# Kernel optimization log

Hardware: AMD Instinct MI355X
Metric: run time of the kernel (lower is better)

Reference implementation:

```python
import jax, jax.numpy as jnp
import numpy as np

N_HEAD = 4
D_K = 512 // N_HEAD  # 128
PAD = 5  # (kernel 11 - 1) // 2, sanm_shift=0 -> symmetric 'same' padding
EPS = 1e-5


def layer_norm(x, w, b):
    m = jnp.mean(x, axis=-1, keepdims=True)
    v = jnp.mean(jnp.square(x - m), axis=-1, keepdims=True)
    return (x - m) * jax.lax.rsqrt(v + EPS) * w + b


def setup_inputs() -> dict:
    key = jax.random.key(0)
    ks = jax.random.split(key, 8)
    B, T, D = 64, 218, 512
    s = 0.05
    return {
        "x": jax.random.normal(ks[0], (B, T, D), jnp.float32),
        "masks": jnp.ones((B, T), jnp.float32),
        "ln0_w": jax.random.uniform(ks[1], (D,), jnp.float32, 0.9, 1.1),
        "ln0_b": jnp.zeros((D,), jnp.float32),
        "ln1_w": jax.random.uniform(ks[2], (D,), jnp.float32, 0.9, 1.1),
        "ln1_b": jnp.zeros((D,), jnp.float32),
        "qkv_w": jax.random.normal(ks[3], (D, 3 * D), jnp.float32) * s,
        "qkv_b": jnp.zeros((3 * D,), jnp.float32),
        "out_w": jax.random.normal(ks[4], (D, D), jnp.float32) * s,
        "out_b": jnp.zeros((D,), jnp.float32),
        "fsmn_w": jax.random.normal(ks[5], (D, D, 11), jnp.float32) * s,
        "w1": jax.random.normal(ks[6], (D, 4 * D), jnp.float32) * s,
        "b1": jnp.zeros((4 * D,), jnp.float32),
        "w2": jax.random.normal(ks[7], (4 * D, D), jnp.float32) * s,
        "b2": jnp.zeros((D,), jnp.float32),
    }


def encoder_layer(x, masks, ln0_w, ln0_b, ln1_w, ln1_b, qkv_w, qkv_b,
                  out_w, out_b, fsmn_w, w1, b1, w2, b2):
    B, T, D = x.shape
    m = masks[..., None]  # (B,T,1)

    # ---- self_attn_sanm block ----
    residual = x
    h = layer_norm(x, ln0_w, ln0_b)
    qkv = h @ qkv_w + qkv_b                      # (B,T,3D)
    q, k, v = jnp.split(qkv, 3, axis=-1)         # each (B,T,D)

    # FSMN memory branch on (masked) v: Conv1d(512,512,11), 'same' padding
    vm = v * m
    # torch conv weight (out,in,k) -> jax 'WIO' kernel (k,in,out)
    kern = jnp.transpose(fsmn_w, (2, 1, 0))
    fsmn = jax.lax.conv_general_dilated(
        vm, kern, window_strides=(1,), padding=[(PAD, PAD)],
        dimension_numbers=("NWC", "WIO", "NWC"))
    fsmn = (fsmn + vm) * m                       # (B,T,D)

    # multi-head attention
    def heads(t):  # (B,T,D) -> (B,H,T,dk)
        return t.reshape(B, T, N_HEAD, D_K).transpose(0, 2, 1, 3)
    qh, kh, vh = heads(q), heads(k), heads(v)
    scores = jnp.einsum("bhqd,bhkd->bhqk", qh, kh) / np.sqrt(D_K)
    neg = jnp.finfo(scores.dtype).min
    scores = jnp.where(masks[:, None, None, :] > 0, scores, neg)
    attn = jax.nn.softmax(scores, axis=-1)
    ctx = jnp.einsum("bhqk,bhkd->bhqd", attn, vh)
    ctx = ctx.transpose(0, 2, 1, 3).reshape(B, T, D)
    att_out = ctx @ out_w + out_b + fsmn
    x = residual + att_out

    # ---- feed-forward block (512 -> 2048 -> 512, relu) ----
    residual = x
    h = layer_norm(x, ln1_w, ln1_b)
    ffn = jax.nn.relu(h @ w1 + b1) @ w2 + b2
    return residual + ffn


def reference(x, masks, ln0_w, ln0_b, ln1_w, ln1_b, qkv_w, qkv_b,
              out_w, out_b, fsmn_w, w1, b1, w2, b2):
    return encoder_layer(x, masks, ln0_w, ln0_b, ln1_w, ln1_b,
                         qkv_w, qkv_b, out_w, out_b, fsmn_w, w1, b1, w2, b2)
```

## Files before the change

kernel.cpp:

```cpp
#include <hip/hip_runtime.h>
#include <cstdint>

#define B_   64
#define T_   218
#define TP_  228
#define D_   512
#define M_   13952
#define MT_  109
#define H_   4
#define DK_  128
#define N3_  1536
#define DFF_ 2048
#define KC_  5632

typedef unsigned short u16;
using short8 = __attribute__((ext_vector_type(8))) short;
using f32x4  = __attribute__((ext_vector_type(4))) float;

__device__ __forceinline__ float b2f(u16 u) {
  union { float f; uint32_t i; } v; v.i = ((uint32_t)u) << 16; return v.f;
}
__device__ __forceinline__ u16 f2b(float f) {
  union { float f; uint32_t i; } v; v.f = f;
  uint32_t r = v.i + 0x7fffu + ((v.i >> 16) & 1u);
  return (u16)(r >> 16);
}
union U8 { uint4 v; u16 u[8]; };

__device__ __forceinline__ void gll16(const u16* g, u16* l) {
  __builtin_amdgcn_global_load_lds(
      (const __attribute__((address_space(1))) unsigned int*)g,
      (__attribute__((address_space(3))) unsigned int*)l, 16, 0, 0);
}


template<int MODE>
__global__ __launch_bounds__(256, 2)
void gemm_u(const u16* __restrict__ A, int sA, const u16* __restrict__ Bt, int sB,
            const float* __restrict__ bias, const u16* __restrict__ convb,
            u16* __restrict__ vmout,
            const float* __restrict__ add_f, void* __restrict__ outp,
            int N, int K, int ntc, const float* __restrict__ masks)
{
  __shared__ u16 As[128 * 32];
  __shared__ u16 Bs[128 * 32];

  const int xcd = blockIdx.x & 7;
  const int lin = blockIdx.x >> 3;
  const int nt = lin % ntc;
  const int mt = xcd + 8 * (lin / ntc);
  if (mt >= MT_) return;
  const int m0 = mt * 128, n0 = nt * 128;

  const int tid = threadIdx.x, lane = tid & 63, w = tid >> 6;
  const int wm = (w >> 1) * 64, wn = (w & 1) * 64;
  const int l15 = lane & 15, qd = lane >> 4;

  const int rl = lane >> 2;
  const int ce = ((lane & 3) ^ ((lane >> 3) & 3)) * 8;
  const int sw8 = (qd ^ ((lane >> 1) & 3)) * 8;
  const int r0 = m0 + w * 16 + rl, r1 = r0 + 64;
  const u16* ag0 = A + (size_t)r0 * sA + ce;
  const u16* ag1 = A + (size_t)r1 * sA + ce;
  const u16* bg0 = Bt + (size_t)(n0 + w * 16 + rl) * sB + ce;
  const u16* bg1 = bg0 + (size_t)64 * sB;
  u16* lA0 = As + w * 512;
  u16* lA1 = As + 2048 + w * 512;
  u16* lB0 = Bs + w * 512;
  u16* lB1 = Bs + 2048 + w * 512;

  const f32x4 z4 = {0.f, 0.f, 0.f, 0.f};
  f32x4 acc[4][4];
#pragma unroll
  for (int i = 0; i < 4; i++)
#pragma unroll
    for (int j = 0; j < 4; j++) acc[i][j] = z4;

  for (int k0 = 0; k0 < K; k0 += 32) {
    __syncthreads();
    gll16(ag0 + k0, lA0);
    gll16(ag1 + k0, lA1);
    gll16(bg0 + k0, lB0);
    gll16(bg1 + k0, lB1);
    __syncthreads();
    short8 af[4], bf[4];
#pragma unroll
    for (int mi = 0; mi < 4; mi++) af[mi] = *(const short8*)&As[(wm + mi * 16 + l15) * 32 + sw8];
#pragma unroll
    for (int ni = 0; ni < 4; ni++) bf[ni] = *(const short8*)&Bs[(wn + ni * 16 + l15) * 32 + sw8];
#pragma unroll
    for (int mi = 0; mi < 4; mi++)
#pragma unroll
      for (int ni = 0; ni < 4; ni++)
        acc[mi][ni] = __builtin_amdgcn_mfma_f32_16x16x32_bf16(af[mi], bf[ni], acc[mi][ni], 0, 0, 0);
  }

#pragma unroll
  for (int ni = 0; ni < 4; ni++) {
    const int c = n0 + wn + ni * 16 + l15;
    const float bv = bias[c];
#pragma unroll
    for (int mi = 0; mi < 4; mi++) {
#pragma unroll
      for (int rg = 0; rg < 4; rg++) {
        const int r = m0 + wm + mi * 16 + qd * 4 + rg;
        float v = acc[mi][ni][rg] + bv;
        if (MODE == 0) {
          ((u16*)outp)[(size_t)r * N + c] = f2b(v);
          if (c >= 1024) {
            const int b = r / T_, t = r - b * T_;
            vmout[((size_t)b * TP_ + t + 5) * D_ + (c - 1024)] = f2b(v * masks[r]);
          }
        } else if (MODE == 1) {
          const size_t idx = (size_t)r * N + c;
          ((float*)outp)[idx] = v + b2f(convb[idx]) + add_f[idx];
        } else if (MODE == 2) {
          ((u16*)outp)[(size_t)r * N + c] = f2b(fmaxf(v, 0.f));
        } else {
          const size_t idx = (size_t)r * N + c;
          ((float*)outp)[idx] = v + add_f[idx];
        }
      }
    }
  }
}

__global__ __launch_bounds__(256, 2)
void conv_gemm(const u16* __restrict__ vmpad, const u16* __restrict__ Wt,
               const float* __restrict__ masks, u16* __restrict__ convb)
{
  __shared__ u16 As[240 * 32];
  __shared__ u16 Bs[11 * 64 * 32];

  const int nt = blockIdx.x & 7, b = blockIdx.x >> 3;
  const int n0 = nt * 64;
  const int base = b * TP_;

  const int tid = threadIdx.x, lane = tid & 63, w = tid >> 6;
  const int wm = (w >> 1) * 112, wn = (w & 1) * 32;
  const int l15 = lane & 15, qd = lane >> 4;
  const int rl = lane >> 2;
  const int ce = ((lane & 3) ^ ((lane >> 3) & 3)) * 8;

  int abase[7];
#pragma unroll
  for (int mi = 0; mi < 7; mi++) abase[mi] = (wm + mi * 16 + l15) * 64;
  int toff[11];
#pragma unroll
  for (int tap = 0; tap < 11; tap++)
    toff[tap] = tap * 64 + ((qd ^ (((l15 + tap) >> 1) & 3)) << 4);
  const int swb8 = (qd ^ ((l15 >> 1) & 3)) * 8;

  const f32x4 z4 = {0.f, 0.f, 0.f, 0.f};
  f32x4 acc[7][2];
#pragma unroll
  for (int i = 0; i < 7; i++) { acc[i][0] = z4; acc[i][1] = z4; }

  for (int kc = 0; kc < 16; kc++) {
    const int kb = kc * 32;
    __syncthreads();
    for (int c = w; c < 15; c += 4)
      gll16(vmpad + (size_t)(base + c * 16 + rl) * D_ + kb + ce, As + c * 512);
    for (int c = w; c < 44; c += 4) {
      const int tap = c >> 2, q = c & 3;
      gll16(Wt + (size_t)(n0 + q * 16 + rl) * KC_ + tap * 512 + kb + ce,
            Bs + c * 512);
    }
    __syncthreads();
    const char* Ab = (const char*)As;
#pragma unroll
    for (int tap = 0; tap < 11; tap++) {
      short8 bf0 = *(const short8*)&Bs[tap * 2048 + (wn + l15) * 32 + swb8];
      short8 bf1 = *(const short8*)&Bs[tap * 2048 + (wn + 16 + l15) * 32 + swb8];
#pragma unroll
      for (int mi = 0; mi < 7; mi++) {
        short8 af = *(const short8*)(Ab + (abase[mi] + toff[tap]));
        acc[mi][0] = __builtin_amdgcn_mfma_f32_16x16x32_bf16(af, bf0, acc[mi][0], 0, 0, 0);
        acc[mi][1] = __builtin_amdgcn_mfma_f32_16x16x32_bf16(af, bf1, acc[mi][1], 0, 0, 0);
      }
    }
  }

#pragma unroll
  for (int mi = 0; mi < 7; mi++) {
#pragma unroll
    for (int rg = 0; rg < 4; rg++) {
      const int rlcl = wm + mi * 16 + qd * 4 + rg;
      if (rlcl < T_) {
        const int r = b * T_ + rlcl;
        const int vrow = base + rlcl + 5;
        const float m = masks[r];
#pragma unroll
        for (int ni = 0; ni < 2; ni++) {
          const int c = n0 + wn + ni * 16 + l15;
          const float vm = b2f(vmpad[(size_t)vrow * D_ + c]);
          convb[(size_t)r * D_ + c] = f2b((acc[mi][ni][rg] + vm) * m);
        }
      }
    }
  }
}

__global__ __launch_bounds__(256, 2)
void attn_fused(const u16* __restrict__ qkv, const float* __restrict__ masks,
                u16* __restrict__ ctx)
{
  __shared__ u16 smem[29696];
  __shared__ float red0[4][64];
  __shared__ float red1[4][64];
  u16* Qs = smem;
  u16* Ks = smem + 64 * 136;
  u16* Ps = smem;
  u16* Vs = smem + 64 * 232;

  const int tid = threadIdx.x, lane = tid & 63, w = tid >> 6;
  const int l15 = lane & 15, qd = lane >> 4;
  const int bh = blockIdx.y, b = bh >> 2, h = bh & 3;
  const int q0 = blockIdx.x * 64;
  const uint4 uz = make_uint4(0, 0, 0, 0);

#pragma unroll
  for (int i = 0; i < 4; i++) {
    const int ch = tid + i * 256;
    const int row = ch >> 4, cg = (ch & 15) * 8;
    const int t = q0 + row;
    uint4 v = uz;
    if (t < T_) v = *(const uint4*)(qkv + ((size_t)b * T_ + t) * N3_ + h * DK_ + cg);
    *(uint4*)&Qs[row * 136 + cg] = v;
  }

  const f32x4 z4 = {0.f, 0.f, 0.f, 0.f};
  f32x4 acc[4][4];
#pragma unroll
  for (int i = 0; i < 4; i++)
#pragma unroll
    for (int j = 0; j < 4; j++) acc[i][j] = z4;

#pragma unroll
  for (int kc = 0; kc < 4; kc++) {
    __syncthreads();
#pragma unroll
    for (int i = 0; i < 4; i++) {
      const int ch = tid + i * 256;
      const int row = ch >> 4, cg = (ch & 15) * 8;
      const int t = kc * 64 + row;
      uint4 v = uz;
      if (t < T_) v = *(const uint4*)(qkv + ((size_t)b * T_ + t) * N3_ + D_ + h * DK_ + cg);
      *(uint4*)&Ks[row * 136 + cg] = v;
    }
    __syncthreads();
#pragma unroll
    for (int ks = 0; ks < 4; ks++) {
      short8 bf = *(const short8*)&Ks[(w * 16 + l15) * 136 + ks * 32 + qd * 8];
#pragma unroll
      for (int mi = 0; mi < 4; mi++) {
        short8 af = *(const short8*)&Qs[(mi * 16 + l15) * 136 + ks * 32 + qd * 8];
        acc[kc][mi] = __builtin_amdgcn_mfma_f32_16x16x32_bf16(af, bf, acc[kc][mi], 0, 0, 0);
      }
    }
  }

  const float scale = 0.08838834764831845f;
  const int colb = w * 16 + l15;
  bool valid[4];
#pragma unroll
  for (int kc = 0; kc < 4; kc++) {
    const int col = kc * 64 + colb;
    valid[kc] = (col < T_) && (masks[b * T_ + col] > 0.f);
  }

  float mx[4][4];
#pragma unroll
  for (int mi = 0; mi < 4; mi++)
#pragma unroll
    for (int rg = 0; rg < 4; rg++) {
      float m = -1e30f;
#pragma unroll
      for (int kc = 0; kc < 4; kc++)
        if (valid[kc]) m = fmaxf(m, acc[kc][mi][rg] * scale);
      for (int d = 1; d < 16; d <<= 1) m = fmaxf(m, __shfl_xor(m, d, 64));
      mx[mi][rg] = m;
    }
  if (l15 == 0) {
#pragma unroll
    for (int mi = 0; mi < 4; mi++)
#pragma unroll
      for (int rg = 0; rg < 4; rg++) red0[w][mi * 16 + qd * 4 + rg] = mx[mi][rg];
  }
  __syncthreads();
#pragma unroll
  for (int mi = 0; mi < 4; mi++)
#pragma unroll
    for (int rg = 0; rg < 4; rg++) {
      const int r = mi * 16 + qd * 4 + rg;
      mx[mi][rg] = fmaxf(fmaxf(red0[0][r], red0[1][r]), fmaxf(red0[2][r], red0[3][r]));
    }
  float sm[4][4];
#pragma unroll
  for (int mi = 0; mi < 4; mi++)
#pragma unroll
    for (int rg = 0; rg < 4; rg++) {
      float s = 0.f;
#pragma unroll
      for (int kc = 0; kc < 4; kc++)
        if (valid[kc]) s += __expf(acc[kc][mi][rg] * scale - mx[mi][rg]);
      for (int d = 1; d < 16; d <<= 1) s += __shfl_xor(s, d, 64);
      sm[mi][rg] = s;
    }
  if (l15 == 0) {
#pragma unroll
    for (int mi = 0; mi < 4; mi++)
#pragma unroll
      for (int rg = 0; rg < 4; rg++) red1[w][mi * 16 + qd * 4 + rg] = sm[mi][rg];
  }
  __syncthreads();
#pragma unroll
  for (int mi = 0; mi < 4; mi++)
#pragma unroll
    for (int rg = 0; rg < 4; rg++) {
      const int r = mi * 16 + qd * 4 + rg;
      const float inv = 1.f / (red1[0][r] + red1[1][r] + red1[2][r] + red1[3][r]);
#pragma unroll
      for (int kc = 0; kc < 4; kc++) {
        const int col = kc * 64 + colb;
        if (col < 224) {
          const float p = valid[kc] ? __expf(acc[kc][mi][rg] * scale - mx[mi][rg]) * inv : 0.f;
          Ps[r * 232 + col] = f2b(p);
        }
      }
    }

  const int kvg = tid >> 4, dg = tid & 15;
#pragma unroll
  for (int half = 0; half < 2; ++half) {
    __syncthreads();
#pragma unroll
    for (int r = 0; r < 14; ++r) {
      const int kv = r * 16 + kvg;
      ushort4 vv = make_ushort4(0, 0, 0, 0);
      if (kv < T_)
        vv = *(const ushort4*)(qkv + ((size_t)b * T_ + kv) * N3_ + 1024 + h * DK_ + half * 64 + dg * 4);
      Vs[(dg * 4 + 0) * 232 + kv] = vv.x;
      Vs[(dg * 4 + 1) * 232 + kv] = vv.y;
      Vs[(dg * 4 + 2) * 232 + kv] = vv.z;
      Vs[(dg * 4 + 3) * 232 + kv] = vv.w;
    }
    __syncthreads();
    f32x4 a2[4] = {z4, z4, z4, z4};
#pragma unroll
    for (int k0 = 0; k0 < 7; ++k0) {
      short8 af = *(const short8*)&Ps[(w * 16 + l15) * 232 + k0 * 32 + qd * 8];
#pragma unroll
      for (int nt = 0; nt < 4; ++nt) {
        short8 bf = *(const short8*)&Vs[(nt * 16 + l15) * 232 + k0 * 32 + qd * 8];
        a2[nt] = __builtin_amdgcn_mfma_f32_16x16x32_bf16(af, bf, a2[nt], 0, 0, 0);
      }
    }
    const int tb = q0 + w * 16 + qd * 4;
#pragma unroll
    for (int nt = 0; nt < 4; ++nt) {
      const int d = h * DK_ + half * 64 + nt * 16 + l15;
#pragma unroll
      for (int rg = 0; rg < 4; ++rg) {
        const int tt = tb + rg;
        if (tt < T_) ctx[((size_t)b * T_ + tt) * D_ + d] = f2b(a2[nt][rg]);
      }
    }
  }
}

__global__ __launch_bounds__(256)
void ln_k(const float* __restrict__ x, const float* __restrict__ wgt,
          const float* __restrict__ bia, u16* __restrict__ outp)
{
  const int lane = threadIdx.x & 63, wv = threadIdx.x >> 6;
  const size_t row = (size_t)blockIdx.x * 4 + wv;
  const float* rp = x + row * D_ + lane * 8;
  float v[8], s = 0.f, s2 = 0.f;
  float4 r0 = *(const float4*)rp;
  float4 r1 = *(const float4*)(rp + 4);
  v[0] = r0.x; v[1] = r0.y; v[2] = r0.z; v[3] = r0.w;
  v[4] = r1.x; v[5] = r1.y; v[6] = r1.z; v[7] = r1.w;
#pragma unroll
  for (int i = 0; i < 8; i++) { s += v[i]; s2 += v[i] * v[i]; }
  for (int d = 1; d < 64; d <<= 1) { s += __shfl_xor(s, d, 64); s2 += __shfl_xor(s2, d, 64); }
  const float mean = s * (1.f / 512.f);
  const float var  = s2 * (1.f / 512.f) - mean * mean;
  const float rs   = rsqrtf(var + 1e-5f);
  float4 w0 = *(const float4*)(wgt + lane * 8);
  float4 w1 = *(const float4*)(wgt + lane * 8 + 4);
  float4 b0 = *(const float4*)(bia + lane * 8);
  float4 b1 = *(const float4*)(bia + lane * 8 + 4);
  const float wv8[8] = {w0.x, w0.y, w0.z, w0.w, w1.x, w1.y, w1.z, w1.w};
  const float bv8[8] = {b0.x, b0.y, b0.z, b0.w, b1.x, b1.y, b1.z, b1.w};
  U8 o;
#pragma unroll
  for (int i = 0; i < 8; i++)
    o.u[i] = f2b((v[i] - mean) * rs * wv8[i] + bv8[i]);
  *(uint4*)(outp + row * D_ + lane * 8) = o.v;
}

__global__ __launch_bounds__(256)
void prep_all(const float* __restrict__ qkv_w, const float* __restrict__ out_w,
              const float* __restrict__ w1, const float* __restrict__ w2,
              const float* __restrict__ fsmn_w,
              u16* __restrict__ qkv_wT, u16* __restrict__ out_wT,
              u16* __restrict__ w1T, u16* __restrict__ w2T,
              u16* __restrict__ fsmnW2, u16* __restrict__ vmpad)
{
  const int bid = blockIdx.x;
  if (bid < 3072) {
    const float* src; u16* dst; int K, N, tb;
    if (bid < 768)       { src = qkv_w; dst = qkv_wT; K = 512;  N = 1536; tb = bid; }
    else if (bid < 1024) { src = out_w; dst = out_wT; K = 512;  N = 512;  tb = bid - 768; }
    else if (bid < 2048) { src = w1;    dst = w1T;    K = 512;  N = 2048; tb = bid - 1024; }
    else                 { src = w2;    dst = w2T;    K = 2048; N = 512;  tb = bid - 2048; }
    const int ktiles = K / 32;
    const int k0 = (tb % ktiles) * 32, n0 = (tb / ktiles) * 32;
    __shared__ float tile[32][33];
    const int x = threadIdx.x & 31, y = threadIdx.x >> 5;
#pragma unroll
    for (int j = 0; j < 4; j++)
      tile[y + j * 8][x] = src[(size_t)(k0 + y + j * 8) * N + n0 + x];
    __syncthreads();
#pragma unroll
    for (int j = 0; j < 4; j++)
      dst[(size_t)(n0 + y + j * 8) * K + k0 + x] = f2b(tile[x][y + j * 8]);
  } else if (bid < 4096) {
    const int idx = (bid - 3072) * 256 + threadIdx.x;
    const int o = idx >> 9, i = idx & 511;
    const float* s = fsmn_w + (size_t)idx * 11;
#pragma unroll
    for (int tap = 0; tap < 11; ++tap)
      fsmnW2[(size_t)o * KC_ + tap * 512 + i] = f2b(s[tap]);
  } else {
    const int e8 = (bid - 4096) * 256 + threadIdx.x;
    const int e  = e8 * 8;
    const int c  = e & 511;
    const int pr = e >> 9;
    int row;
    if (pr < 640) {
      const int b = pr / 10, j = pr % 10;
      row = b * TP_ + ((j < 5) ? j : (218 + j));
    } else {
      row = B_ * TP_ + (pr - 640);
    }
    *(uint4*)(vmpad + (size_t)row * D_ + c) = make_uint4(0, 0, 0, 0);
  }
}

extern "C" void kernel_launch(void* const* d_in, const int* in_sizes, int n_in,
                              void* d_out, int out_size, void* d_ws, size_t ws_size,
                              hipStream_t stream)
{
  const float* x      = (const float*)d_in[0];
  const float* masks  = (const float*)d_in[1];
  const float* ln0_w  = (const float*)d_in[2];
  const float* ln0_b  = (const float*)d_in[3];
  const float* ln1_w  = (const float*)d_in[4];
  const float* ln1_b  = (const float*)d_in[5];
  const float* qkv_w  = (const float*)d_in[6];
  const float* qkv_b  = (const float*)d_in[7];
  const float* out_w  = (const float*)d_in[8];
  const float* out_b  = (const float*)d_in[9];
  const float* fsmn_w = (const float*)d_in[10];
  const float* w1     = (const float*)d_in[11];
  const float* b1     = (const float*)d_in[12];
  const float* w2     = (const float*)d_in[13];
  const float* b2     = (const float*)d_in[14];
  float* outp = (float*)d_out;
  u16* ws   = (u16*)d_ws;

  size_t off = 0;
  u16* qkv_wT = ws + off; off += (size_t)1536 * 512;
  u16* out_wT = ws + off; off += (size_t)512 * 512;
  u16* w1T    = ws + off; off += (size_t)2048 * 512;
  u16* w2T    = ws + off; off += (size_t)512 * 2048;
  u16* fsmnW2 = ws + off; off += (size_t)512 * KC_;
  u16* slotA  = ws + off; off += (size_t)M_ * 512;
  u16* qkvb   = ws + off; off += (size_t)M_ * 1536;
  u16* vmpad  = ws + off; off += (size_t)(B_ * TP_ + 320) * 512;
  u16* regionX= ws + off;
  u16* convb  = regionX;
  u16* hid    = regionX;
  u16* h1     = qkvb;
  float* x1   = (float*)(qkvb + (size_t)M_ * 512);

  prep_all<<<4126, 256, 0, stream>>>(qkv_w, out_w, w1, w2, fsmn_w,
                                     qkv_wT, out_wT, w1T, w2T, fsmnW2, vmpad);
  ln_k<<<M_ / 4, 256, 0, stream>>>(x, ln0_w, ln0_b, slotA);
  gemm_u<0><<<8 * 14 * 12, 256, 0, stream>>>(
      slotA, 512, qkv_wT, 512, qkv_b, nullptr, vmpad, nullptr, qkvb,
      1536, 512, 12, masks);
  conv_gemm<<<512, 256, 0, stream>>>(vmpad, fsmnW2, masks, convb);
  attn_fused<<<dim3(4, 256), 256, 0, stream>>>(qkvb, masks, slotA);
  gemm_u<1><<<8 * 14 * 4, 256, 0, stream>>>(
      slotA, 512, out_wT, 512, out_b, convb, nullptr, x, x1,
      512, 512, 4, masks);
  ln_k<<<M_ / 4, 256, 0, stream>>>(x1, ln1_w, ln1_b, h1);
  gemm_u<2><<<8 * 14 * 16, 256, 0, stream>>>(
      h1, 512, w1T, 512, b1, nullptr, nullptr, nullptr, hid,
      2048, 512, 16, nullptr);
  gemm_u<3><<<8 * 14 * 4, 256, 0, stream>>>(
      hid, 2048, w2T, 2048, b2, nullptr, nullptr, x1, outp,
      512, 2048, 4, nullptr);
}
```

Before: 443.6 us.

## Double-buffer conv_gemm LDS tiles and use 8 waves per block

The FSMN conv GEMM kernel now uses two LDS buffers so the global-to-LDS loads for the next K-chunk are issued while MFMAs run on the current one, leaving one barrier per iteration instead of two. The block grows from 256 to 512 threads, so each wave computes a 16-column slice instead of 32, halving per-wave accumulators. The cost is roughly double the LDS footprint (about 120 KB per block), which can limit blocks per CU, and each wave reloads the same A fragments for fewer MFMAs.

```diff
diff --git a/kernel.cpp b/kernel.cpp
--- a/kernel.cpp
+++ b/kernel.cpp
@@ -125,19 +125,18 @@
   }
 }
 
-__global__ __launch_bounds__(256, 2)
+__global__ __launch_bounds__(512, 2)
 void conv_gemm(const u16* __restrict__ vmpad, const u16* __restrict__ Wt,
                const float* __restrict__ masks, u16* __restrict__ convb)
 {
-  __shared__ u16 As[240 * 32];
-  __shared__ u16 Bs[11 * 64 * 32];
+  __shared__ u16 smem[2][30208];
 
   const int nt = blockIdx.x & 7, b = blockIdx.x >> 3;
   const int n0 = nt * 64;
   const int base = b * TP_;
 
   const int tid = threadIdx.x, lane = tid & 63, w = tid >> 6;
-  const int wm = (w >> 1) * 112, wn = (w & 1) * 32;
+  const int wm = (w >> 2) * 112, wn = (w & 3) * 16;
   const int l15 = lane & 15, qd = lane >> 4;
   const int rl = lane >> 2;
   const int ce = ((lane & 3) ^ ((lane >> 3) & 3)) * 8;
@@ -152,34 +151,44 @@
   const int swb8 = (qd ^ ((l15 >> 1) & 3)) * 8;
 
   const f32x4 z4 = {0.f, 0.f, 0.f, 0.f};
-  f32x4 acc[7][2];
-#pragma unroll
-  for (int i = 0; i < 7; i++) { acc[i][0] = z4; acc[i][1] = z4; }
+  f32x4 acc[7];
+#pragma unroll
+  for (int i = 0; i < 7; i++) acc[i] = z4;
+
+#define STAGE(kc, bufi)                                                        \
+  {                                                                            \
+    const int kb = (kc) * 32;                                                  \
+    u16* Ab_ = smem[bufi];                                                     \
+    u16* Bb_ = smem[bufi] + 7680;                                              \
+    for (int c = w; c < 15; c += 8)                                            \
+      gll16(vmpad + (size_t)(base + c * 16 + rl) * D_ + kb + ce, Ab_ + c * 512);\
+    for (int c = w; c < 44; c += 8) {                                          \
+      const int tap_ = c >> 2, q_ = c & 3;                                     \
+      gll16(Wt + (size_t)(n0 + q_ * 16 + rl) * KC_ + tap_ * 512 + kb + ce,     \
+            Bb_ + c * 512);                                                    \
+    }                                                                          \
+  }
+
+  STAGE(0, 0);
+  __syncthreads();
 
   for (int kc = 0; kc < 16; kc++) {
-    const int kb = kc * 32;
-    __syncthreads();
-    for (int c = w; c < 15; c += 4)
-      gll16(vmpad + (size_t)(base + c * 16 + rl) * D_ + kb + ce, As + c * 512);
-    for (int c = w; c < 44; c += 4) {
-      const int tap = c >> 2, q = c & 3;
-      gll16(Wt + (size_t)(n0 + q * 16 + rl) * KC_ + tap * 512 + kb + ce,
-            Bs + c * 512);
-    }
-    __syncthreads();
-    const char* Ab = (const char*)As;
+    const int cur = kc & 1;
+    if (kc < 15) STAGE(kc + 1, cur ^ 1);
+    const char* Ab = (const char*)smem[cur];
+    const u16* Bb = smem[cur] + 7680;
 #pragma unroll
     for (int tap = 0; tap < 11; tap++) {
-      short8 bf0 = *(const short8*)&Bs[tap * 2048 + (wn + l15) * 32 + swb8];
-      short8 bf1 = *(const short8*)&Bs[tap * 2048 + (wn + 16 + l15) * 32 + swb8];
+      short8 bf = *(const short8*)&Bb[tap * 2048 + (wn + l15) * 32 + swb8];
 #pragma unroll
       for (int mi = 0; mi < 7; mi++) {
         short8 af = *(const short8*)(Ab + (abase[mi] + toff[tap]));
-        acc[mi][0] = __builtin_amdgcn_mfma_f32_16x16x32_bf16(af, bf0, acc[mi][0], 0, 0, 0);
-        acc[mi][1] = __builtin_amdgcn_mfma_f32_16x16x32_bf16(af, bf1, acc[mi][1], 0, 0, 0);
-      }
-    }
-  }
+        acc[mi] = __builtin_amdgcn_mfma_f32_16x16x32_bf16(af, bf, acc[mi], 0, 0, 0);
+      }
+    }
+    __syncthreads();
+  }
+#undef STAGE
 
 #pragma unroll
   for (int mi = 0; mi < 7; mi++) {
@@ -190,12 +199,9 @@
         const int r = b * T_ + rlcl;
         const int vrow = base + rlcl + 5;
         const float m = masks[r];
-#pragma unroll
-        for (int ni = 0; ni < 2; ni++) {
-          const int c = n0 + wn + ni * 16 + l15;
-          const float vm = b2f(vmpad[(size_t)vrow * D_ + c]);
-          convb[(size_t)r * D_ + c] = f2b((acc[mi][ni][rg] + vm) * m);
-        }
+        const int c = n0 + wn + l15;
+        const float vm = b2f(vmpad[(size_t)vrow * D_ + c]);
+        convb[(size_t)r * D_ + c] = f2b((acc[mi][rg] + vm) * m);
       }
     }
   }
@@ -492,7 +498,7 @@
   gemm_u<0><<<8 * 14 * 12, 256, 0, stream>>>(
       slotA, 512, qkv_wT, 512, qkv_b, nullptr, vmpad, nullptr, qkvb,
       1536, 512, 12, masks);
-  conv_gemm<<<512, 256, 0, stream>>>(vmpad, fsmnW2, masks, convb);
+  conv_gemm<<<512, 512, 0, stream>>>(vmpad, fsmnW2, masks, convb);
   attn_fused<<<dim3(4, 256), 256, 0, stream>>>(qkvb, masks, slotA);
   gemm_u<1><<<8 * 14 * 4, 256, 0, stream>>>(
       slotA, 512, out_wT, 512, out_b, convb, nullptr, x, x1,
```

Measured after the change: 468.7 us. 1.06x slower.
